# Optimization experiments

Measured on AMD Instinct MI355X. Metric: run time of the kernel, lower is better.

Reference implementation:

```python
import jax, jax.numpy as jnp
import numpy as np

EMBED_DIM = 1024
N_HEAD = 16
HEAD_DIM = EMBED_DIM // N_HEAD


def setup_inputs() -> dict:
    key = jax.random.key(0)
    k1, k2, k3 = jax.random.split(key, 3)
    B, S = 2, 2048
    x = jax.random.normal(k1, (B, S, EMBED_DIM), dtype=jnp.float32)
    # kaiming-style scale for the packed QKV projection and output projection
    w_qkv = jax.random.normal(k2, (3 * EMBED_DIM, EMBED_DIM), dtype=jnp.float32) * np.sqrt(2.0 / EMBED_DIM)
    w0 = jax.random.normal(k3, (EMBED_DIM, EMBED_DIM), dtype=jnp.float32) * np.sqrt(2.0 / EMBED_DIM)
    return {"x": x, "w_qkv": w_qkv, "w0": w0}


def reference(x, w_qkv, w0):
    B, S, E = x.shape
    # fused QKV projection (Linear with no bias): x @ w_qkv.T -> [B,S,3E]
    qkv = jnp.einsum('bse,fe->bsf', x, w_qkv)
    q, k, v = jnp.split(qkv, 3, axis=-1)
    # reshape to [B, H, S, D]
    def heads(t):
        return t.reshape(B, S, N_HEAD, HEAD_DIM).transpose(0, 2, 1, 3)
    q, k, v = heads(q), heads(k), heads(v)
    scale = 1.0 / np.sqrt(HEAD_DIM).astype(np.float32)
    scores = jnp.einsum('bhsd,bhtd->bhst', q, k) * scale  # [B,H,S,S]
    # causal additive bias: -inf above the diagonal (same math as the precomputed bias tensor)
    causal = jnp.tril(jnp.ones((S, S), dtype=bool))
    scores = jnp.where(causal, scores, -jnp.inf)
    probs = jax.nn.softmax(scores, axis=-1)
    e = jnp.einsum('bhst,bhtd->bhsd', probs, v)  # [B,H,S,D]
    e = e.transpose(0, 2, 1, 3).reshape(B, S, E)
    # output projection: E @ w0.T
    return jnp.einsum('bse,fe->bsf', e, w0)
```

## Files before the change

### kernel.cpp

```cpp
#include <hip/hip_runtime.h>


typedef unsigned short u16;
typedef short bf16x8 __attribute__((ext_vector_type(8)));
typedef float f32x4 __attribute__((ext_vector_type(4)));
typedef unsigned short u16x4 __attribute__((ext_vector_type(4)));

#define S_LEN 2048
#define EMB 1024
#define NH 16
#define HD 64
#define QKV_W 3072
#define BATCH 2
#define CSC 0.18033688f
#define PSTR 72

static __device__ __forceinline__ u16 f2bf(float f) {
    unsigned x = __float_as_uint(f);
    return (u16)((x + 0x7fffu + ((x >> 16) & 1u)) >> 16);
}

static __device__ __forceinline__ void gld_lds16(const u16* g, u16* l) {
    __builtin_amdgcn_global_load_lds(
        (const __attribute__((address_space(1))) void*)g,
        (__attribute__((address_space(3))) void*)l, 16, 0, 0);
}

#define XN4 (BATCH * S_LEN * EMB / 4)
#define WQ4 (QKV_W * EMB / 4)
#define W04 (EMB * EMB / 4)
__global__ __launch_bounds__(256) void cvt_all(const float* __restrict__ x,
                                               const float* __restrict__ wq,
                                               const float* __restrict__ w0,
                                               u16* __restrict__ xb,
                                               u16* __restrict__ wqb,
                                               u16* __restrict__ w0b) {
    int i = blockIdx.x * 256 + threadIdx.x;
    const float* src;
    u16* dst;
    int off;
    if (i < XN4) { src = x; dst = xb; off = i; }
    else if (i < XN4 + WQ4) { src = wq; dst = wqb; off = i - XN4; }
    else { src = w0; dst = w0b; off = i - XN4 - WQ4; }
    float4 v = ((const float4*)src)[off];
    u16x4 o;
    o[0] = f2bf(v.x); o[1] = f2bf(v.y); o[2] = f2bf(v.z); o[3] = f2bf(v.w);
    ((u16x4*)dst)[off] = o;
}

template <typename OutT, int BN>
__global__ __launch_bounds__(256) void gemm_bt(const u16* __restrict__ A,
                                               const u16* __restrict__ Bt,
                                               OutT* __restrict__ C,
                                               int M, int N, int K, int qcols) {
    constexpr int NF = BN / 32;
    __shared__ alignas(16) u16 As[128 * 32];
    __shared__ alignas(16) u16 Bs[BN * 32];
    const int tid = threadIdx.x;
    const int wave = tid >> 6, lane = tid & 63;
    const int quad = lane >> 4, lr = lane & 15;
    const int m0 = blockIdx.y * 128, n0 = blockIdx.x * BN;
    const int wm = (wave & 1) * 64, wn = (wave >> 1) * (BN / 2);
    const float sc = (n0 < qcols) ? CSC : 1.0f;

    f32x4 acc[4][NF] = {};

    for (int k0 = 0; k0 < K; k0 += 32) {
#pragma unroll
        for (int i = 0; i < 2; ++i) {
            int chunk = tid + i * 256;
            int row = chunk >> 2;
            int col8 = (chunk & 3) * 8;
            gld_lds16(&A[(size_t)(m0 + row) * K + k0 + col8], &As[row * 32 + col8]);
        }
#pragma unroll
        for (int i = 0; i < BN / 64; ++i) {
            int chunk = tid + i * 256;
            int row = chunk >> 2;
            int col8 = (chunk & 3) * 8;
            gld_lds16(&Bt[(size_t)(n0 + row) * K + k0 + col8], &Bs[row * 32 + col8]);
        }
        __syncthreads();
        bf16x8 af[4], bf[NF];
#pragma unroll
        for (int i = 0; i < 4; ++i)
            af[i] = *(const bf16x8*)&As[(wm + i * 16 + lr) * 32 + quad * 8];
#pragma unroll
        for (int i = 0; i < NF; ++i)
            bf[i] = *(const bf16x8*)&Bs[(wn + i * 16 + lr) * 32 + quad * 8];
#pragma unroll
        for (int mi = 0; mi < 4; ++mi)
#pragma unroll
            for (int ni = 0; ni < NF; ++ni)
                acc[mi][ni] = __builtin_amdgcn_mfma_f32_16x16x32_bf16(
                    af[mi], bf[ni], acc[mi][ni], 0, 0, 0);
        __syncthreads();
    }

#pragma unroll
    for (int mi = 0; mi < 4; ++mi) {
#pragma unroll
        for (int r = 0; r < 4; ++r) {
            int gr = m0 + wm + mi * 16 + quad * 4 + r;
#pragma unroll
            for (int ni = 0; ni < NF; ++ni) {
                int gc = n0 + wn + ni * 16 + lr;
                float v = acc[mi][ni][r] * sc;
                if constexpr (sizeof(OutT) == 2)
                    C[(size_t)gr * N + gc] = (OutT)f2bf(v);
                else
                    C[(size_t)gr * N + gc] = (OutT)v;
            }
        }
    }
}

__global__ __launch_bounds__(256) void transpose_v(const u16* __restrict__ qkv,
                                                   u16* __restrict__ vt) {
    __shared__ alignas(16) u16 t[64][72];
    const int s0 = blockIdx.x * 64;
    const int bh = blockIdx.y;
    const int b = bh >> 4, h = bh & 15;
#pragma unroll
    for (int i = 0; i < 2; ++i) {
        int chunk = threadIdx.x + i * 256;
        int row = chunk >> 3;
        int c8 = (chunk & 7) * 8;
        uint4 v = *(const uint4*)&qkv[(size_t)(b * S_LEN + s0 + row) * QKV_W +
                                      2 * EMB + h * HD + c8];
        const u16* p = (const u16*)&v;
#pragma unroll
        for (int jj = 0; jj < 8; ++jj) t[c8 + jj][row] = p[jj];
    }
    __syncthreads();
#pragma unroll
    for (int i = 0; i < 2; ++i) {
        int chunk = threadIdx.x + i * 256;
        int d = chunk >> 3;
        int c8 = (chunk & 7) * 8;
        uint4 v = *(const uint4*)&t[d][c8];
        *(uint4*)&vt[((size_t)bh * HD + d) * S_LEN + s0 + c8] = v;
    }
}

__global__ __launch_bounds__(512, 4) void attn(const u16* __restrict__ qkv,
                                               const u16* __restrict__ vt,
                                               u16* __restrict__ e) {
    const int tid = threadIdx.x;
    const int w = tid >> 6, lane = tid & 63;
    const int quad = lane >> 4, lr = lane & 15;
    const int pi = blockIdx.x;
    const int qtB = 31 - pi;
    const int bh = blockIdx.y, b = bh >> 4, h = bh & 15;
    const int myqt = (w < 4) ? pi : qtB;
    const int qbase = myqt * 64 + (w & 3) * 16;

    __shared__ alignas(16) u16 Ks[2 * 2 * 64 * 32];
    __shared__ alignas(16) u16 Vs[2 * 2 * 64 * 32];
    __shared__ alignas(16) u16 plds[8][16 * PSTR];
    u16* pw = plds[w];

    const u16* qkv_b = qkv + (size_t)b * S_LEN * QKV_W;
    const u16* qrow = qkv_b + (size_t)(qbase + lr) * QKV_W + h * HD + quad * 8;
    const bf16x8 qf0 = *(const bf16x8*)(qrow);
    const bf16x8 qf1 = *(const bf16x8*)(qrow + 32);

    const u16* kbase = qkv_b + EMB + h * HD;
    const u16* vbase = vt + (size_t)bh * HD * S_LEN;

    f32x4 o[4] = {};
    float lsum = 0.f;
    const int qg = qbase + lr;

    const int sr = (w & 3) * 16 + (lane >> 2);
    const int sc = (lane & 3) * 8;

    auto stage = [&](int j, int bb) {
        const int kv0 = j * 64;
        if (w < 4) {
            gld_lds16(kbase + (size_t)(kv0 + sr) * QKV_W + sc,
                      &Ks[bb * 4096 + sr * 32 + sc]);
            gld_lds16(kbase + (size_t)(kv0 + sr) * QKV_W + 32 + sc,
                      &Ks[bb * 4096 + 2048 + sr * 32 + sc]);
        } else {
            gld_lds16(vbase + (size_t)sr * S_LEN + kv0 + sc,
                      &Vs[bb * 4096 + sr * 32 + sc]);
            gld_lds16(vbase + (size_t)sr * S_LEN + kv0 + 32 + sc,
                      &Vs[bb * 4096 + 2048 + sr * 32 + sc]);
        }
    };

    stage(0, 0);
    for (int j = 0; j <= qtB; ++j) {
        const int bb = j & 1;
        __syncthreads();
        if (j < qtB) stage(j + 1, 1 - bb);
        if (j <= myqt) {
            const int kv0 = j * 64;
            const u16* ks = &Ks[bb * 4096];
            const u16* vs = &Vs[bb * 4096];
            f32x4 s[4];
#pragma unroll
            for (int nt = 0; nt < 4; ++nt) {
                bf16x8 k0 = *(const bf16x8*)&ks[(nt * 16 + lr) * 32 + quad * 8];
                bf16x8 k1 = *(const bf16x8*)&ks[2048 + (nt * 16 + lr) * 32 + quad * 8];
                f32x4 z = {};
                z = __builtin_amdgcn_mfma_f32_16x16x32_bf16(k0, qf0, z, 0, 0, 0);
                z = __builtin_amdgcn_mfma_f32_16x16x32_bf16(k1, qf1, z, 0, 0, 0);
                s[nt] = z;
            }
            const bool diag = (j == myqt);
            __builtin_amdgcn_wave_barrier();
#pragma unroll
            for (int nt = 0; nt < 4; ++nt) {
                float p[4];
#pragma unroll
                for (int r = 0; r < 4; ++r) {
                    float pv = exp2f(s[nt][r]);
                    if (diag) pv = (kv0 + nt * 16 + quad * 4 + r > qg) ? 0.f : pv;
                    p[r] = pv;
                }
                lsum += (p[0] + p[1]) + (p[2] + p[3]);
                uint2 pk;
                pk.x = __builtin_amdgcn_perm(__float_as_uint(p[1]),
                                             __float_as_uint(p[0]), 0x07060302u);
                pk.y = __builtin_amdgcn_perm(__float_as_uint(p[3]),
                                             __float_as_uint(p[2]), 0x07060302u);
                *(uint2*)&pw[lr * PSTR + nt * 16 + quad * 4] = pk;
            }
            __builtin_amdgcn_wave_barrier();
            const bf16x8 p0 = *(const bf16x8*)&pw[lr * PSTR + quad * 8];
            const bf16x8 p1 = *(const bf16x8*)&pw[lr * PSTR + 32 + quad * 8];
#pragma unroll
            for (int nt = 0; nt < 4; ++nt) {
                bf16x8 v0 = *(const bf16x8*)&vs[(nt * 16 + lr) * 32 + quad * 8];
                bf16x8 v1 = *(const bf16x8*)&vs[2048 + (nt * 16 + lr) * 32 + quad * 8];
                o[nt] = __builtin_amdgcn_mfma_f32_16x16x32_bf16(p0, v0, o[nt], 0, 0, 0);
                o[nt] = __builtin_amdgcn_mfma_f32_16x16x32_bf16(p1, v1, o[nt], 0, 0, 0);
            }
        }
    }

    float lf = lsum + __shfl_xor(lsum, 16, 64);
    lf += __shfl_xor(lf, 32, 64);
#pragma unroll
    for (int r = 0; r < 4; ++r) {
        float inv = 1.0f / __shfl(lf, quad * 4 + r, 64);
        size_t row = (size_t)(b * S_LEN + qbase + quad * 4 + r) * EMB + h * HD;
#pragma unroll
        for (int nt = 0; nt < 4; ++nt)
            e[row + nt * 16 + lr] = f2bf(o[nt][r] * inv);
    }
}

extern "C" void kernel_launch(void* const* d_in, const int* in_sizes, int n_in,
                              void* d_out, int out_size, void* d_ws, size_t ws_size,
                              hipStream_t stream) {
    const float* x = (const float*)d_in[0];
    const float* w_qkv = (const float*)d_in[1];
    const float* w0 = (const float*)d_in[2];
    float* out = (float*)d_out;

    const size_t M = (size_t)BATCH * S_LEN;
    u16* xb = (u16*)d_ws;
    u16* wqb = xb + M * EMB;
    u16* w0b = wqb + (size_t)QKV_W * EMB;
    u16* qkvb = w0b + (size_t)EMB * EMB;
    u16* vtb = qkvb + M * QKV_W;
    u16* eb = vtb + (size_t)BATCH * NH * HD * S_LEN;

    cvt_all<<<(XN4 + WQ4 + W04) / 256, 256, 0, stream>>>(x, w_qkv, w0, xb, wqb, w0b);

    gemm_bt<u16, 128><<<dim3(QKV_W / 128, M / 128), 256, 0, stream>>>(
        xb, wqb, qkvb, (int)M, QKV_W, EMB, EMB);

    transpose_v<<<dim3(S_LEN / 64, BATCH * NH), 256, 0, stream>>>(qkvb, vtb);

    attn<<<dim3(16, BATCH * NH), 512, 0, stream>>>(qkvb, vtb, eb);

    gemm_bt<float, 64><<<dim3(EMB / 64, M / 128), 256, 0, stream>>>(
        eb, w0b, out, (int)M, EMB, EMB, 0);
}
```

Before: 189.3 us.

## Switch attention to 32x32x16 MFMA with 4-wave blocks and swizzled LDS

The attention kernel now uses 32x32x16 bf16 MFMA tiles, so each wave handles 32 query rows instead of 16, and blocks shrink from 8 waves to 4. Loading K/V tiles into LDS uses an XOR swizzle on column groups to avoid bank conflicts, and every thread stages both K and V. Block-to-head mapping is permuted to balance causal work across the grid. The larger tiles raise MFMA efficiency and cut LDS traffic per FLOP, at the cost of more registers per wave and fewer waves per block.

Measured after the change: 209.4 us. 10.6% more time.

```diff
diff --git a/kernel.cpp b/kernel.cpp
--- a/kernel.cpp
+++ b/kernel.cpp
@@ -4,6 +4,7 @@
 typedef unsigned short u16;
 typedef short bf16x8 __attribute__((ext_vector_type(8)));
 typedef float f32x4 __attribute__((ext_vector_type(4)));
+typedef float f32x16 __attribute__((ext_vector_type(16)));
 typedef unsigned short u16x4 __attribute__((ext_vector_type(4)));
 
 #define S_LEN 2048
@@ -143,51 +144,50 @@
     }
 }
 
-__global__ __launch_bounds__(512, 4) void attn(const u16* __restrict__ qkv,
+__global__ __launch_bounds__(256, 2) void attn(const u16* __restrict__ qkv,
                                                const u16* __restrict__ vt,
                                                u16* __restrict__ e) {
     const int tid = threadIdx.x;
     const int w = tid >> 6, lane = tid & 63;
-    const int quad = lane >> 4, lr = lane & 15;
-    const int pi = blockIdx.x;
+    const int lo = lane & 31, hi = lane >> 5;
+    const int bx = blockIdx.x, by = blockIdx.y;
+    const int flip = (by >> 4) & 1;
+    const int pi = flip ? (15 - bx) : bx;
+    const int bh = ((by & 15) << 1) | flip;
     const int qtB = 31 - pi;
-    const int bh = blockIdx.y, b = bh >> 4, h = bh & 15;
-    const int myqt = (w < 4) ? pi : qtB;
-    const int qbase = myqt * 64 + (w & 3) * 16;
-
-    __shared__ alignas(16) u16 Ks[2 * 2 * 64 * 32];
-    __shared__ alignas(16) u16 Vs[2 * 2 * 64 * 32];
-    __shared__ alignas(16) u16 plds[8][16 * PSTR];
+    const int b = bh >> 4, h = bh & 15;
+    const int myqt = (w < 2) ? pi : qtB;
+    const int qb = myqt * 64 + (w & 1) * 32;
+
+    __shared__ alignas(16) u16 Ks[2][4096];
+    __shared__ alignas(16) u16 Vs[2][4096];
+    __shared__ alignas(16) u16 plds[4][32 * PSTR];
     u16* pw = plds[w];
 
     const u16* qkv_b = qkv + (size_t)b * S_LEN * QKV_W;
-    const u16* qrow = qkv_b + (size_t)(qbase + lr) * QKV_W + h * HD + quad * 8;
-    const bf16x8 qf0 = *(const bf16x8*)(qrow);
-    const bf16x8 qf1 = *(const bf16x8*)(qrow + 32);
+    const u16* qrow = qkv_b + (size_t)(qb + lo) * QKV_W + h * HD;
+    bf16x8 qf[4];
+#pragma unroll
+    for (int s = 0; s < 4; ++s) qf[s] = *(const bf16x8*)(qrow + s * 16 + hi * 8);
 
     const u16* kbase = qkv_b + EMB + h * HD;
     const u16* vbase = vt + (size_t)bh * HD * S_LEN;
 
-    f32x4 o[4] = {};
+    f32x16 oacc[2] = {};
     float lsum = 0.f;
-    const int qg = qbase + lr;
-
-    const int sr = (w & 3) * 16 + (lane >> 2);
-    const int sc = (lane & 3) * 8;
+    const int qg = qb + lo;
+
+    const int srow = tid >> 2;
+    const int scg = ((tid & 3) ^ (srow & 3)) * 8;
 
     auto stage = [&](int j, int bb) {
         const int kv0 = j * 64;
-        if (w < 4) {
-            gld_lds16(kbase + (size_t)(kv0 + sr) * QKV_W + sc,
-                      &Ks[bb * 4096 + sr * 32 + sc]);
-            gld_lds16(kbase + (size_t)(kv0 + sr) * QKV_W + 32 + sc,
-                      &Ks[bb * 4096 + 2048 + sr * 32 + sc]);
-        } else {
-            gld_lds16(vbase + (size_t)sr * S_LEN + kv0 + sc,
-                      &Vs[bb * 4096 + sr * 32 + sc]);
-            gld_lds16(vbase + (size_t)sr * S_LEN + kv0 + 32 + sc,
-                      &Vs[bb * 4096 + 2048 + sr * 32 + sc]);
-        }
+        gld_lds16(kbase + (size_t)(kv0 + srow) * QKV_W + scg, &Ks[bb][tid * 8]);
+        gld_lds16(kbase + (size_t)(kv0 + srow) * QKV_W + 32 + scg,
+                  &Ks[bb][2048 + tid * 8]);
+        gld_lds16(vbase + (size_t)srow * S_LEN + kv0 + scg, &Vs[bb][tid * 8]);
+        gld_lds16(vbase + (size_t)srow * S_LEN + kv0 + 32 + scg,
+                  &Vs[bb][2048 + tid * 8]);
     };
 
     stage(0, 0);
@@ -197,59 +197,83 @@
         if (j < qtB) stage(j + 1, 1 - bb);
         if (j <= myqt) {
             const int kv0 = j * 64;
-            const u16* ks = &Ks[bb * 4096];
-            const u16* vs = &Vs[bb * 4096];
-            f32x4 s[4];
-#pragma unroll
-            for (int nt = 0; nt < 4; ++nt) {
-                bf16x8 k0 = *(const bf16x8*)&ks[(nt * 16 + lr) * 32 + quad * 8];
-                bf16x8 k1 = *(const bf16x8*)&ks[2048 + (nt * 16 + lr) * 32 + quad * 8];
-                f32x4 z = {};
-                z = __builtin_amdgcn_mfma_f32_16x16x32_bf16(k0, qf0, z, 0, 0, 0);
-                z = __builtin_amdgcn_mfma_f32_16x16x32_bf16(k1, qf1, z, 0, 0, 0);
-                s[nt] = z;
+            const u16* ks = Ks[bb];
+            const u16* vs = Vs[bb];
+            f32x16 sac[2];
+#pragma unroll
+            for (int ntk = 0; ntk < 2; ++ntk) {
+                f32x16 z = {};
+#pragma unroll
+                for (int s = 0; s < 4; ++s) {
+                    int cg = s * 2 + hi;
+                    int row = ntk * 32 + lo;
+                    bf16x8 kf = *(const bf16x8*)&ks[(cg >> 2) * 2048 + row * 32 +
+                                                    (((cg & 3) ^ (row & 3)) * 8)];
+                    z = __builtin_amdgcn_mfma_f32_32x32x16_bf16(kf, qf[s], z, 0, 0, 0);
+                }
+                sac[ntk] = z;
             }
             const bool diag = (j == myqt);
             __builtin_amdgcn_wave_barrier();
 #pragma unroll
-            for (int nt = 0; nt < 4; ++nt) {
-                float p[4];
-#pragma unroll
-                for (int r = 0; r < 4; ++r) {
-                    float pv = exp2f(s[nt][r]);
-                    if (diag) pv = (kv0 + nt * 16 + quad * 4 + r > qg) ? 0.f : pv;
-                    p[r] = pv;
+            for (int ntk = 0; ntk < 2; ++ntk) {
+#pragma unroll
+                for (int g = 0; g < 4; ++g) {
+                    float p[4];
+#pragma unroll
+                    for (int rr = 0; rr < 4; ++rr) {
+                        int kv = kv0 + ntk * 32 + 8 * g + 4 * hi + rr;
+                        float pv = exp2f(sac[ntk][g * 4 + rr]);
+                        if (diag) pv = (kv > qg) ? 0.f : pv;
+                        p[rr] = pv;
+                    }
+                    lsum += (p[0] + p[1]) + (p[2] + p[3]);
+                    uint2 pk;
+                    pk.x = __builtin_amdgcn_perm(__float_as_uint(p[1]),
+                                                 __float_as_uint(p[0]), 0x07060302u);
+                    pk.y = __builtin_amdgcn_perm(__float_as_uint(p[3]),
+                                                 __float_as_uint(p[2]), 0x07060302u);
+                    *(uint2*)&pw[lo * PSTR + ntk * 32 + 8 * g + 4 * hi] = pk;
                 }
-                lsum += (p[0] + p[1]) + (p[2] + p[3]);
-                uint2 pk;
-                pk.x = __builtin_amdgcn_perm(__float_as_uint(p[1]),
-                                             __float_as_uint(p[0]), 0x07060302u);
-                pk.y = __builtin_amdgcn_perm(__float_as_uint(p[3]),
-                                             __float_as_uint(p[2]), 0x07060302u);
-                *(uint2*)&pw[lr * PSTR + nt * 16 + quad * 4] = pk;
             }
             __builtin_amdgcn_wave_barrier();
-            const bf16x8 p0 = *(const bf16x8*)&pw[lr * PSTR + quad * 8];
-            const bf16x8 p1 = *(const bf16x8*)&pw[lr * PSTR + 32 + quad * 8];
-#pragma unroll
-            for (int nt = 0; nt < 4; ++nt) {
-                bf16x8 v0 = *(const bf16x8*)&vs[(nt * 16 + lr) * 32 + quad * 8];
-                bf16x8 v1 = *(const bf16x8*)&vs[2048 + (nt * 16 + lr) * 32 + quad * 8];
-                o[nt] = __builtin_amdgcn_mfma_f32_16x16x32_bf16(p0, v0, o[nt], 0, 0, 0);
-                o[nt] = __builtin_amdgcn_mfma_f32_16x16x32_bf16(p1, v1, o[nt], 0, 0, 0);
-            }
-        }
-    }
-
-    float lf = lsum + __shfl_xor(lsum, 16, 64);
-    lf += __shfl_xor(lf, 32, 64);
-#pragma unroll
-    for (int r = 0; r < 4; ++r) {
-        float inv = 1.0f / __shfl(lf, quad * 4 + r, 64);
-        size_t row = (size_t)(b * S_LEN + qbase + quad * 4 + r) * EMB + h * HD;
-#pragma unroll
-        for (int nt = 0; nt < 4; ++nt)
-            e[row + nt * 16 + lr] = f2bf(o[nt][r] * inv);
+            bf16x8 pf[4];
+#pragma unroll
+            for (int s2 = 0; s2 < 4; ++s2)
+                pf[s2] = *(const bf16x8*)&pw[lo * PSTR + s2 * 16 + hi * 8];
+#pragma unroll
+            for (int ntd = 0; ntd < 2; ++ntd) {
+#pragma unroll
+                for (int s2 = 0; s2 < 4; ++s2) {
+                    int cg = s2 * 2 + hi;
+                    int row = ntd * 32 + lo;
+                    bf16x8 vf = *(const bf16x8*)&vs[(cg >> 2) * 2048 + row * 32 +
+                                                    (((cg & 3) ^ (row & 3)) * 8)];
+                    oacc[ntd] = __builtin_amdgcn_mfma_f32_32x32x16_bf16(
+                        pf[s2], vf, oacc[ntd], 0, 0, 0);
+                }
+            }
+        }
+    }
+
+    float lf = lsum + __shfl_xor(lsum, 32, 64);
+    float inv[4][4];
+#pragma unroll
+    for (int g = 0; g < 4; ++g)
+#pragma unroll
+        for (int rr = 0; rr < 4; ++rr)
+            inv[g][rr] = 1.0f / __shfl(lf, rr + 8 * g + 4 * hi, 64);
+#pragma unroll
+    for (int ntd = 0; ntd < 2; ++ntd) {
+#pragma unroll
+        for (int g = 0; g < 4; ++g) {
+#pragma unroll
+            for (int rr = 0; rr < 4; ++rr) {
+                int ql = rr + 8 * g + 4 * hi;
+                size_t row = (size_t)(b * S_LEN + qb + ql) * EMB + h * HD;
+                e[row + ntd * 32 + lo] = f2bf(oacc[ntd][g * 4 + rr] * inv[g][rr]);
+            }
+        }
     }
 }
 
@@ -276,7 +300,7 @@
 
     transpose_v<<<dim3(S_LEN / 64, BATCH * NH), 256, 0, stream>>>(qkvb, vtb);
 
-    attn<<<dim3(16, BATCH * NH), 512, 0, stream>>>(qkvb, vtb, eb);
+    attn<<<dim3(16, BATCH * NH), 256, 0, stream>>>(qkvb, vtb, eb);
 
     gemm_bt<float, 64><<<dim3(EMB / 64, M / 128), 256, 0, stream>>>(
         eb, w0b, out, (int)M, EMB, EMB, 0);
```
